# Kernel tuning notes

Hardware: AMD Instinct MI355X
Metric: run time of the kernel (lower is better)

Reference implementation:

```python
import jax, jax.numpy as jnp
import numpy as np

NUM_CLUSTERS = 64
DIM = 256
EPS = 1e-12  # torch F.normalize eps


def setup_inputs() -> dict:
    key = jax.random.key(0)
    k1, k2, k3, k4 = jax.random.split(key, 4)
    x = jax.random.normal(k1, (128, DIM, 32, 32), dtype=jnp.float32)
    # nn.Conv2d(256, K, 1) params: weight (K, C, 1, 1) -> store as (K, C); bias (K,)
    fan_in = DIM
    bound = 1.0 / np.sqrt(fan_in)
    conv_w = jax.random.uniform(k2, (NUM_CLUSTERS, DIM), jnp.float32, -bound, bound)
    conv_b = jax.random.uniform(k3, (NUM_CLUSTERS,), jnp.float32, -bound, bound)
    centroids = jax.random.uniform(k4, (NUM_CLUSTERS, DIM), jnp.float32)  # torch.rand
    return {"x": x, "conv_w": conv_w, "conv_b": conv_b, "centroids": centroids}


def _l2norm(v, axis):
    n = jnp.sqrt(jnp.sum(v * v, axis=axis, keepdims=True))
    return v / jnp.maximum(n, EPS)


def reference(x, conv_w, conv_b, centroids):
    N, C, H, W = x.shape
    K = conv_w.shape[0]
    # L2-normalize over channel dim
    x = _l2norm(x, axis=1)                      # (N, C, H, W)
    xf = x.reshape(N, C, H * W)                 # (N, C, P)
    # 1x1 conv == per-pixel linear over channels
    logits = jnp.einsum('ncp,kc->nkp', xf, conv_w) + conv_b[None, :, None]
    a = jax.nn.softmax(logits, axis=1)          # (N, K, P) softmax over clusters
    # VLAD via matmul decomposition: sum_p a[n,k,p]*(x[n,:,p] - c[k,:])
    agg = jnp.einsum('nkp,ncp->nkc', a, xf)     # (N, K, C)
    asum = jnp.sum(a, axis=-1)                  # (N, K)
    vlad = agg - asum[:, :, None] * centroids[None, :, :]
    vlad = _l2norm(vlad, axis=2)                # intra-normalization
    vlad = vlad.reshape(N, K * C)
    return _l2norm(vlad, axis=1)
```

## Files before the change

### kernel.cpp

```cpp
#include <hip/hip_runtime.h>
#include <math.h>


#define EPSF 1e-12f

typedef __attribute__((ext_vector_type(8))) __bf16 bf16x8;
typedef __attribute__((ext_vector_type(4))) float f32x4;
typedef __attribute__((ext_vector_type(4))) unsigned int u32x4;

#define MFMA(a, b, c) __builtin_amdgcn_mfma_f32_16x16x32_bf16((a), (b), (c), 0, 0, 0)

__device__ __forceinline__ bf16x8 as_bf(u32x4 v) { return __builtin_bit_cast(bf16x8, v); }

__device__ __forceinline__ unsigned packsplit(float x) {
    const unsigned u  = __float_as_uint(x);
    const unsigned hi = u & 0xFFFF0000u;
    const float lof   = x - __uint_as_float(hi);
    return hi | (__float_as_uint(lof) >> 16);
}

struct u32pair { unsigned h, l; };

__device__ __forceinline__ u32pair splitpair(float f0, float f1) {
    const unsigned u0 = __float_as_uint(f0), u1 = __float_as_uint(f1);
    u32pair r;
    r.h = __builtin_amdgcn_perm(u1, u0, 0x07060302u);
    const float l0 = f0 - __uint_as_float(u0 & 0xFFFF0000u);
    const float l1 = f1 - __uint_as_float(u1 & 0xFFFF0000u);
    r.l = __builtin_amdgcn_perm(__float_as_uint(l1), __float_as_uint(l0), 0x07060302u);
    return r;
}

__device__ __forceinline__ void unpack2q(const u32x4 q0, const u32x4 q1,
                                         u32x4& hi, u32x4& lo) {
    hi[0] = __builtin_amdgcn_perm(q0[1], q0[0], 0x07060302u);
    lo[0] = __builtin_amdgcn_perm(q0[1], q0[0], 0x05040100u);
    hi[1] = __builtin_amdgcn_perm(q0[3], q0[2], 0x07060302u);
    lo[1] = __builtin_amdgcn_perm(q0[3], q0[2], 0x05040100u);
    hi[2] = __builtin_amdgcn_perm(q1[1], q1[0], 0x07060302u);
    lo[2] = __builtin_amdgcn_perm(q1[1], q1[0], 0x05040100u);
    hi[3] = __builtin_amdgcn_perm(q1[3], q1[2], 0x07060302u);
    lo[3] = __builtin_amdgcn_perm(q1[3], q1[2], 0x05040100u);
}

__device__ __forceinline__ void split8v(const float* xv, u32x4& hi, u32x4& lo) {
    #pragma unroll
    for (int w2 = 0; w2 < 4; ++w2) {
        const u32pair r = splitpair(xv[2*w2], xv[2*w2+1]);
        hi[w2] = r.h;
        lo[w2] = r.l;
    }
}

__global__ void split_w_kernel(const float* __restrict__ wmat,
                               unsigned* __restrict__ whiG,
                               unsigned* __restrict__ wloG) {
    const int idx = blockIdx.x * 256 + threadIdx.x;
    const int mt = idx >> 9, s = (idx >> 6) & 7, l = idx & 63;
    const int k = mt * 16 + (l & 15);
    const int cb = s * 32 + 8 * (l >> 4);
    const float* wr = wmat + k * 256 + cb;
    const float4 f0 = *(const float4*)wr;
    const float4 f1 = *(const float4*)(wr + 4);
    const float xv[8] = {f0.x, f0.y, f0.z, f0.w, f1.x, f1.y, f1.z, f1.w};
    u32x4 hi, lo; split8v(xv, hi, lo);
    *(u32x4*)(whiG + idx * 4) = hi;
    *(u32x4*)(wloG + idx * 4) = lo;
}

__global__ __launch_bounds__(256, 4) void netvlad_p1(
    const float* __restrict__ x,
    const unsigned* __restrict__ whiG, const unsigned* __restrict__ wloG,
    const float* __restrict__ bias, unsigned* __restrict__ aG,
    float* __restrict__ asum_part) {

    __shared__ float asum_lds[4][64];
    const int t = threadIdx.x;
    const int w = t >> 6, l = t & 63;
    const int l15 = l & 15, lg4 = l >> 4;
    const int n = blockIdx.x & 127, e = blockIdx.x >> 7;
    const size_t ximg = (size_t)n * 256 * 1024;
    const int p0 = e * 128;
    const int cs = lg4 * 8;

    f32x4 acc1[4][2];
    #pragma unroll
    for (int i = 0; i < 4; ++i) {
        acc1[i][0] = f32x4{0.f, 0.f, 0.f, 0.f};
        acc1[i][1] = f32x4{0.f, 0.f, 0.f, 0.f};
    }
    float ssa[2] = {0.f, 0.f};

    #define P1_ADDR(st_) (x + ximg + (size_t)(((st_) >> 1) * 32 + cs) * 1024 \
                          + p0 + (2 * w + ((st_) & 1)) * 16 + l15)
    float nxv[8];
    {
        const float* bp = P1_ADDR(0);
        #pragma unroll
        for (int j = 0; j < 8; ++j) nxv[j] = bp[(size_t)j * 1024];
    }
    u32x4 wh[4], wl[4];
    #pragma unroll
    for (int st = 0; st < 16; ++st) {
        const int s = st >> 1, ntl = st & 1;
        float xv[8];
        #pragma unroll
        for (int j = 0; j < 8; ++j) xv[j] = nxv[j];
        if (st < 15) {
            const float* bp = P1_ADDR(st + 1);
            #pragma unroll
            for (int j = 0; j < 8; ++j) nxv[j] = bp[(size_t)j * 1024];
        }
        if (ntl == 0) {
            #pragma unroll
            for (int mt = 0; mt < 4; ++mt) {
                const int fo = ((mt * 8 + s) * 64 + l) * 4;
                wh[mt] = *(const u32x4*)(whiG + fo);
                wl[mt] = *(const u32x4*)(wloG + fo);
            }
        }
        #pragma unroll
        for (int j = 0; j < 8; ++j) ssa[ntl] = fmaf(xv[j], xv[j], ssa[ntl]);
        u32x4 bhi, blo; split8v(xv, bhi, blo);
        #pragma unroll
        for (int mt = 0; mt < 4; ++mt) {
            acc1[mt][ntl] = MFMA(as_bf(wh[mt]), as_bf(bhi), acc1[mt][ntl]);
            acc1[mt][ntl] = MFMA(as_bf(wh[mt]), as_bf(blo), acc1[mt][ntl]);
            acc1[mt][ntl] = MFMA(as_bf(wl[mt]), as_bf(bhi), acc1[mt][ntl]);
        }
    }
    #pragma unroll
    for (int ntl = 0; ntl < 2; ++ntl) {
        ssa[ntl] += __shfl_xor(ssa[ntl], 16);
        ssa[ntl] += __shfl_xor(ssa[ntl], 32);
    }

    f32x4 biasv[4];
    #pragma unroll
    for (int mt = 0; mt < 4; ++mt)
        biasv[mt] = *(const f32x4*)(bias + mt * 16 + 4 * lg4);

    float asum_loc[16];
    #pragma unroll
    for (int i = 0; i < 16; ++i) asum_loc[i] = 0.f;

    #pragma unroll
    for (int ntl = 0; ntl < 2; ++ntl) {
        const int p = p0 + (2 * w + ntl) * 16 + l15;
        const float rn = 1.f / fmaxf(sqrtf(ssa[ntl]), EPSF);
        float lgv[16];
        #pragma unroll
        for (int mt = 0; mt < 4; ++mt)
            #pragma unroll
            for (int r = 0; r < 4; ++r)
                lgv[mt * 4 + r] = fmaf(acc1[mt][ntl][r], rn, biasv[mt][r]);
        float mx = lgv[0];
        #pragma unroll
        for (int i = 1; i < 16; ++i) mx = fmaxf(mx, lgv[i]);
        mx = fmaxf(mx, __shfl_xor(mx, 16));
        mx = fmaxf(mx, __shfl_xor(mx, 32));
        float den = 0.f;
        #pragma unroll
        for (int i = 0; i < 16; ++i) { lgv[i] = __expf(lgv[i] - mx); den += lgv[i]; }
        den += __shfl_xor(den, 16);
        den += __shfl_xor(den, 32);
        const float inv = 1.f / den;
        #pragma unroll
        for (int mt = 0; mt < 4; ++mt)
            #pragma unroll
            for (int r = 0; r < 4; ++r) {
                const float av = lgv[mt * 4 + r] * inv;
                asum_loc[mt * 4 + r] += av;
                aG[((size_t)n * 64 + mt * 16 + 4 * lg4 + r) * 1024 + p] =
                    packsplit(av * rn);
            }
    }

    #pragma unroll
    for (int i = 0; i < 16; ++i) {
        float s = asum_loc[i];
        s += __shfl_xor(s, 1);
        s += __shfl_xor(s, 2);
        s += __shfl_xor(s, 4);
        s += __shfl_xor(s, 8);
        if (l15 == 0) asum_lds[w][(i >> 2) * 16 + 4 * lg4 + (i & 3)] = s;
    }
    __syncthreads();
    if (t < 64)
        asum_part[((size_t)n * 8 + e) * 64 + t] =
            asum_lds[0][t] + asum_lds[1][t] + asum_lds[2][t] + asum_lds[3][t];
}

__global__ __launch_bounds__(256, 4) void netvlad_p2(
    const float* __restrict__ x, const unsigned* __restrict__ aG,
    float* __restrict__ out0, float* __restrict__ out1) {

    __shared__ __align__(16) unsigned xs[2][2048];
    __shared__ __align__(16) unsigned as2[2][2048];

    const int t = threadIdx.x;
    const int w = t >> 6, l = t & 63;
    const int l15 = l & 15, lg4 = l >> 4;
    const int n = blockIdx.x & 127;
    const int z = blockIdx.x >> 7;
    const int cq = z & 3, ph = z >> 2;
    const size_t ximg = (size_t)n * 256 * 1024;
    const int c0 = cq * 64;
    const int pb0 = ph * 512;

    const float* srcx[2];
    const unsigned* srca[2];
    unsigned ldsq[2];
    #pragma unroll
    for (int i = 0; i < 2; ++i) {
        const int Q = w * 128 + i * 64 + l;
        const int row = Q >> 3, q = Q & 7;
        const int qs = q ^ (row & 7);
        srcx[i] = x + ximg + (size_t)(c0 + row) * 1024 + pb0 + qs * 4;
        srca[i] = aG + ((size_t)n * 64 + row) * 1024 + pb0 + qs * 4;
        ldsq[i] = (unsigned)((w * 128 + i * 64) * 4);
    }

    #define P2DMA(s_, b_) { _Pragma("unroll")                                 \
        for (int i = 0; i < 2; ++i) {                                         \
            __builtin_amdgcn_global_load_lds(                                 \
                (const __attribute__((address_space(1))) void*)(srcx[i] + (s_) * 32), \
                (__attribute__((address_space(3))) void*)(&xs[b_][ldsq[i]]),  \
                16, 0, 0);                                                    \
            __builtin_amdgcn_global_load_lds(                                 \
                (const __attribute__((address_space(1))) void*)(srca[i] + (s_) * 32), \
                (__attribute__((address_space(3))) void*)(&as2[b_][ldsq[i]]), \
                16, 0, 0);                                                    \
        } }

    f32x4 acc[4];
    #pragma unroll
    for (int mt = 0; mt < 4; ++mt) acc[mt] = f32x4{0.f, 0.f, 0.f, 0.f};

    const int sA = (((lg4 * 2)     ^ (l15 & 7)) << 2);
    const int sB = (((lg4 * 2 + 1) ^ (l15 & 7)) << 2);
    const int rx = w * 16 + l15;

    P2DMA(0, 0);
    #pragma unroll
    for (int ks = 0; ks < 16; ++ks) {
        __syncthreads();
        if (ks < 15) P2DMA(ks + 1, (ks + 1) & 1);
        const unsigned* xb = xs[ks & 1];
        const unsigned* ab = as2[ks & 1];

        const u32x4 fx0 = *(const u32x4*)(xb + rx * 32 + sA);
        const u32x4 fx1 = *(const u32x4*)(xb + rx * 32 + sB);
        float xv[8];
        xv[0] = __uint_as_float(fx0[0]); xv[1] = __uint_as_float(fx0[1]);
        xv[2] = __uint_as_float(fx0[2]); xv[3] = __uint_as_float(fx0[3]);
        xv[4] = __uint_as_float(fx1[0]); xv[5] = __uint_as_float(fx1[1]);
        xv[6] = __uint_as_float(fx1[2]); xv[7] = __uint_as_float(fx1[3]);
        u32x4 bhi, blo; split8v(xv, bhi, blo);

        #pragma unroll
        for (int mt = 0; mt < 4; ++mt) {
            const int ra = mt * 16 + l15;
            const u32x4 pa  = *(const u32x4*)(ab + ra * 32 + sA);
            const u32x4 pbq = *(const u32x4*)(ab + ra * 32 + sB);
            u32x4 ahi, alo; unpack2q(pa, pbq, ahi, alo);
            acc[mt] = MFMA(as_bf(ahi), as_bf(bhi), acc[mt]);
            acc[mt] = MFMA(as_bf(ahi), as_bf(blo), acc[mt]);
            acc[mt] = MFMA(as_bf(alo), as_bf(bhi), acc[mt]);
        }
    }

    float* op = (ph ? out1 : out0) + (size_t)n * 16384;
    #pragma unroll
    for (int mt = 0; mt < 4; ++mt)
        #pragma unroll
        for (int r = 0; r < 4; ++r)
            op[(mt * 16 + 4 * lg4 + r) * 256 + c0 + w * 16 + l15] = acc[mt][r];
}

__global__ __launch_bounds__(256) void netvlad_epi(
    float* __restrict__ out, const float* __restrict__ out1,
    const float* __restrict__ asum_part, const float* __restrict__ cent) {
    __shared__ float wred[4];
    __shared__ float gs_sh;
    const int n = blockIdx.x;
    const int t = threadIdx.x;
    const int k = t >> 2;
    const int q = t & 3;
    float* op = out + (size_t)n * 16384 + k * 256 + q * 64;
    const float* o1 = out1 + (size_t)n * 16384 + k * 256 + q * 64;
    const float* cp = cent + k * 256 + q * 64;
    float as = 0.f;
    #pragma unroll
    for (int e2 = 0; e2 < 8; ++e2)
        as += asum_part[((size_t)n * 8 + e2) * 64 + k];

    float v[64];
    float ss = 0.f;
    #pragma unroll
    for (int i = 0; i < 64; i += 4) {
        const float4 a0 = *(const float4*)&op[i];
        const float4 a1 = *(const float4*)&o1[i];
        const float4 cv = *(const float4*)&cp[i];
        v[i+0] = fmaf(-as, cv.x, a0.x + a1.x);
        v[i+1] = fmaf(-as, cv.y, a0.y + a1.y);
        v[i+2] = fmaf(-as, cv.z, a0.z + a1.z);
        v[i+3] = fmaf(-as, cv.w, a0.w + a1.w);
        ss = fmaf(v[i+0], v[i+0], ss);
        ss = fmaf(v[i+1], v[i+1], ss);
        ss = fmaf(v[i+2], v[i+2], ss);
        ss = fmaf(v[i+3], v[i+3], ss);
    }
    ss += __shfl_xor(ss, 1);
    ss += __shfl_xor(ss, 2);
    const float iscale = 1.f / fmaxf(sqrtf(ss), EPSF);

    float gsum = (q == 0) ? ss * iscale * iscale : 0.f;
    #pragma unroll
    for (int off = 4; off < 64; off <<= 1) gsum += __shfl_xor(gsum, off);
    if ((t & 63) == 0) wred[t >> 6] = gsum;
    __syncthreads();
    if (t == 0) {
        const float tot = wred[0] + wred[1] + wred[2] + wred[3];
        gs_sh = 1.f / fmaxf(sqrtf(tot), EPSF);
    }
    __syncthreads();
    const float fs = iscale * gs_sh;
    #pragma unroll
    for (int i = 0; i < 64; i += 4) {
        float4 w4;
        w4.x = v[i+0] * fs; w4.y = v[i+1] * fs;
        w4.z = v[i+2] * fs; w4.w = v[i+3] * fs;
        *(float4*)&op[i] = w4;
    }
}

extern "C" void kernel_launch(void* const* d_in, const int* in_sizes, int n_in,
                              void* d_out, int out_size, void* d_ws, size_t ws_size,
                              hipStream_t stream) {
    (void)in_sizes; (void)n_in; (void)out_size; (void)ws_size;
    const float* x    = (const float*)d_in[0];
    const float* wmat = (const float*)d_in[1];
    const float* b    = (const float*)d_in[2];
    const float* cent = (const float*)d_in[3];
    float* out = (float*)d_out;
    unsigned* whiG = (unsigned*)d_ws;
    unsigned* wloG = whiG + 8192;
    float* asum_part = (float*)(whiG + 16384);
    unsigned* aG   = whiG + 16384 + 65536;
    float* out1    = (float*)(aG + 8388608);

    split_w_kernel<<<8, 256, 0, stream>>>(wmat, whiG, wloG);
    netvlad_p1<<<1024, 256, 0, stream>>>(x, whiG, wloG, b, aG, asum_part);
    netvlad_p2<<<1024, 256, 0, stream>>>(x, aG, out, out1);
    netvlad_epi<<<128, 256, 0, stream>>>(out, out1, asum_part, cent);
}
```

Baseline: 81.84 us.

## Stage x tiles into LDS via async global_load_lds double buffering in phase 1

Phase 1 no longer does strided per-thread scalar global loads of x with register prefetch. It uses global_load_lds DMA of 16-byte chunks into a swizzled, double-buffered LDS tile, with a __syncthreads per channel slab. Threads then read their 8 channel values from LDS. The aim is coalesced, wider global reads that overlap with MFMA work. The cost is 32KB of LDS per block, which may reduce occupancy, plus extra barriers.

```diff
diff --git a/kernel.cpp b/kernel.cpp
--- a/kernel.cpp
+++ b/kernel.cpp
@@ -74,6 +74,7 @@
     const float* __restrict__ bias, unsigned* __restrict__ aG,
     float* __restrict__ asum_part) {
 
+    __shared__ __align__(16) unsigned xs1[2][4096];
     __shared__ float asum_lds[4][64];
     const int t = threadIdx.x;
     const int w = t >> 6, l = t & 63;
@@ -83,6 +84,22 @@
     const int p0 = e * 128;
     const int cs = lg4 * 8;
 
+    const float* src1[4];
+    unsigned dst1[4];
+    #pragma unroll
+    for (int i = 0; i < 4; ++i) {
+        const int rr = (w * 4 + i) * 2 + (l >> 5);
+        const int psrc = ((l & 31) * 4) ^ (((rr >> 3) & 1) << 4);
+        src1[i] = x + ximg + (size_t)rr * 1024 + p0 + psrc;
+        dst1[i] = (unsigned)((w * 4 + i) * 256);
+    }
+    #define P1DMA(s_, b_) { _Pragma("unroll")                                 \
+        for (int i = 0; i < 4; ++i)                                           \
+            __builtin_amdgcn_global_load_lds(                                 \
+                (const __attribute__((address_space(1))) void*)(src1[i] + (size_t)(s_) * 32768), \
+                (__attribute__((address_space(3))) void*)(&xs1[b_][dst1[i]]), \
+                16, 0, 0); }
+
     f32x4 acc1[4][2];
     #pragma unroll
     for (int i = 0; i < 4; ++i) {
@@ -90,43 +107,37 @@
         acc1[i][1] = f32x4{0.f, 0.f, 0.f, 0.f};
     }
     float ssa[2] = {0.f, 0.f};
-
-    #define P1_ADDR(st_) (x + ximg + (size_t)(((st_) >> 1) * 32 + cs) * 1024 \
-                          + p0 + (2 * w + ((st_) & 1)) * 16 + l15)
-    float nxv[8];
-    {
-        const float* bp = P1_ADDR(0);
-        #pragma unroll
-        for (int j = 0; j < 8; ++j) nxv[j] = bp[(size_t)j * 1024];
-    }
+    const int swzf = (lg4 & 1) << 4;
+
+    P1DMA(0, 0);
     u32x4 wh[4], wl[4];
     #pragma unroll
-    for (int st = 0; st < 16; ++st) {
-        const int s = st >> 1, ntl = st & 1;
-        float xv[8];
-        #pragma unroll
-        for (int j = 0; j < 8; ++j) xv[j] = nxv[j];
-        if (st < 15) {
-            const float* bp = P1_ADDR(st + 1);
-            #pragma unroll
-            for (int j = 0; j < 8; ++j) nxv[j] = bp[(size_t)j * 1024];
+    for (int s = 0; s < 8; ++s) {
+        __syncthreads();
+        if (s < 7) P1DMA(s + 1, (s + 1) & 1);
+        #pragma unroll
+        for (int mt = 0; mt < 4; ++mt) {
+            const int fo = ((mt * 8 + s) * 64 + l) * 4;
+            wh[mt] = *(const u32x4*)(whiG + fo);
+            wl[mt] = *(const u32x4*)(wloG + fo);
         }
-        if (ntl == 0) {
+        const unsigned* xb = xs1[s & 1];
+        #pragma unroll
+        for (int ntl = 0; ntl < 2; ++ntl) {
+            const int colr = (((2 * w + ntl) * 16 + l15) ^ swzf);
+            float xv[8];
+            #pragma unroll
+            for (int j = 0; j < 8; ++j)
+                xv[j] = __uint_as_float(xb[(cs + j) * 128 + colr]);
+            #pragma unroll
+            for (int j = 0; j < 8; ++j) ssa[ntl] = fmaf(xv[j], xv[j], ssa[ntl]);
+            u32x4 bhi, blo; split8v(xv, bhi, blo);
             #pragma unroll
             for (int mt = 0; mt < 4; ++mt) {
-                const int fo = ((mt * 8 + s) * 64 + l) * 4;
-                wh[mt] = *(const u32x4*)(whiG + fo);
-                wl[mt] = *(const u32x4*)(wloG + fo);
+                acc1[mt][ntl] = MFMA(as_bf(wh[mt]), as_bf(bhi), acc1[mt][ntl]);
+                acc1[mt][ntl] = MFMA(as_bf(wh[mt]), as_bf(blo), acc1[mt][ntl]);
+                acc1[mt][ntl] = MFMA(as_bf(wl[mt]), as_bf(bhi), acc1[mt][ntl]);
             }
-        }
-        #pragma unroll
-        for (int j = 0; j < 8; ++j) ssa[ntl] = fmaf(xv[j], xv[j], ssa[ntl]);
-        u32x4 bhi, blo; split8v(xv, bhi, blo);
-        #pragma unroll
-        for (int mt = 0; mt < 4; ++mt) {
-            acc1[mt][ntl] = MFMA(as_bf(wh[mt]), as_bf(bhi), acc1[mt][ntl]);
-            acc1[mt][ntl] = MFMA(as_bf(wh[mt]), as_bf(blo), acc1[mt][ntl]);
-            acc1[mt][ntl] = MFMA(as_bf(wl[mt]), as_bf(bhi), acc1[mt][ntl]);
         }
     }
     #pragma unroll
```

Measured after the change: 81.92 us. No clear change (+0.1%).
